# Performance work log

Measured on AMD Instinct MI355X. Metric: run time of the kernel, lower is better.

Reference implementation:

```python
import jax, jax.numpy as jnp
import numpy as np

NF = 64   # num_feat
DG = 8    # deformable_groups (also conv groups)
B, H, W = 4, 96, 96
K = 9     # 3x3 kernel positions


def _conv(x, w, b, padding=1, dilation=1, groups=1):
    out = jax.lax.conv_general_dilated(
        x, w, (1, 1), [(padding, padding), (padding, padding)],
        rhs_dilation=(dilation, dilation),
        dimension_numbers=('NCHW', 'OIHW', 'NCHW'),
        feature_group_count=groups)
    return out + b[None, :, None, None]


def _lrelu(t):
    return jnp.where(t >= 0, t, 0.1 * t)


def _cat_align(a, b):
    # channel-interleaved concat: [a0,b0,a1,b1,...]
    Bn, k, h, w = a.shape
    return jnp.stack([a, b], axis=2).reshape(Bn, 2 * k, h, w)


def _deform_conv(x, offset, mask, weight, bias, dilation, padding):
    # DCNv2 modulated deformable conv, stride 1.
    Bn, C, h, w = x.shape
    Cpg = C // DG
    off = offset.reshape(Bn, DG, K, 2, h, w)          # (dy, dx) per group/kernel pos
    m = mask.reshape(Bn, DG, K, h, w)
    ky = (jnp.repeat(jnp.arange(3), 3) * dilation - padding).astype(x.dtype)  # (K,)
    kx = (jnp.tile(jnp.arange(3), 3) * dilation - padding).astype(x.dtype)
    hs = jnp.arange(h, dtype=x.dtype)
    ws = jnp.arange(w, dtype=x.dtype)
    py = off[:, :, :, 0] + ky[None, None, :, None, None] + hs[None, None, None, :, None]
    px = off[:, :, :, 1] + kx[None, None, :, None, None] + ws[None, None, None, None, :]
    y0f = jnp.floor(py); x0f = jnp.floor(px)
    ly = (py - y0f)[:, :, None]  # broadcast over Cpg
    lx = (px - x0f)[:, :, None]
    y0 = y0f.astype(jnp.int32); x0 = x0f.astype(jnp.int32)
    xg = x.reshape(Bn, DG, Cpg, h * w)

    def gather(yi, xi):
        inb = ((yi >= 0) & (yi < h) & (xi >= 0) & (xi < w))
        idx = (jnp.clip(yi, 0, h - 1) * w + jnp.clip(xi, 0, w - 1)).reshape(Bn, DG, 1, K * h * w)
        v = jnp.take_along_axis(xg, jnp.broadcast_to(idx, (Bn, DG, Cpg, K * h * w)), axis=3)
        return v.reshape(Bn, DG, Cpg, K, h, w) * inb[:, :, None].astype(x.dtype)

    v00 = gather(y0, x0); v01 = gather(y0, x0 + 1)
    v10 = gather(y0 + 1, x0); v11 = gather(y0 + 1, x0 + 1)
    val = (v00 * (1 - ly) * (1 - lx) + v01 * (1 - ly) * lx
           + v10 * ly * (1 - lx) + v11 * ly * lx) * m[:, :, None]
    sampled = val.reshape(Bn, C, K, h, w)
    out = jnp.einsum('bckhw,ock->bohw', sampled, weight.reshape(weight.shape[0], C, K))
    return out + bias[None, :, None, None]


def _dcn(x, off_feat, om_w, om_b, w, b, dilation):
    pad = dilation  # int(3/2)*dilation
    out = _conv(off_feat, om_w, om_b, padding=pad, dilation=dilation)
    o1, o2, msk = jnp.split(out, 3, axis=1)
    offset = jnp.concatenate([o1, o2], axis=1)
    mask = jax.nn.sigmoid(msk)
    return _deform_conv(x, offset, mask, w, b, dilation, pad)


def setup_inputs() -> dict:
    key = jax.random.key(0)
    ks = iter(jax.random.split(key, 64))
    def rn(shape, s=0.05):
        return jax.random.normal(next(ks), shape, jnp.float32) * s
    d = {}
    d['nbr_feat'] = jax.random.normal(next(ks), (B, NF, H, W), jnp.float32)
    d['ref_feat'] = jax.random.normal(next(ks), (B, NF, H, W), jnp.float32)
    for lv, has3 in [('l3', False), ('l2', True), ('l1', True)]:
        d[f'oc1_w_{lv}'] = rn((NF, 2 * NF // DG, 3, 3)); d[f'oc1_b_{lv}'] = rn((NF,))
        oc2_in = 2 * NF if has3 else NF
        d[f'oc2_w_{lv}'] = rn((NF, oc2_in // DG, 3, 3)); d[f'oc2_b_{lv}'] = rn((NF,))
        if has3:
            d[f'oc3_w_{lv}'] = rn((NF, NF // DG, 3, 3)); d[f'oc3_b_{lv}'] = rn((NF,))
            d[f'fc_w_{lv}'] = rn((NF, 2 * NF // DG, 3, 3)); d[f'fc_b_{lv}'] = rn((NF,))
        d[f'om_w_{lv}'] = rn((DG * 3 * K, NF, 3, 3), 0.01); d[f'om_b_{lv}'] = rn((DG * 3 * K,), 0.01)
        d[f'dcn_w_{lv}'] = rn((NF, NF, 3, 3)); d[f'dcn_b_{lv}'] = rn((NF,))
    d['cas_oc1_w'] = rn((NF, 2 * NF // DG, 3, 3)); d['cas_oc1_b'] = rn((NF,))
    d['cas_oc2_w'] = rn((NF, NF // DG, 3, 3)); d['cas_oc2_b'] = rn((NF,))
    d['cas_om_w'] = rn((DG * 3 * K, NF, 3, 3), 0.01); d['cas_om_b'] = rn((DG * 3 * K,), 0.01)
    d['cas_w'] = rn((NF, NF, 3, 3)); d['cas_b'] = rn((NF,))
    return d


def reference(nbr_feat, ref_feat,
              oc1_w_l3, oc1_b_l3, oc2_w_l3, oc2_b_l3, om_w_l3, om_b_l3, dcn_w_l3, dcn_b_l3,
              oc1_w_l2, oc1_b_l2, oc2_w_l2, oc2_b_l2, oc3_w_l2, oc3_b_l2, fc_w_l2, fc_b_l2,
              om_w_l2, om_b_l2, dcn_w_l2, dcn_b_l2,
              oc1_w_l1, oc1_b_l1, oc2_w_l1, oc2_b_l1, oc3_w_l1, oc3_b_l1, fc_w_l1, fc_b_l1,
              om_w_l1, om_b_l1, dcn_w_l1, dcn_b_l1,
              cas_oc1_w, cas_oc1_b, cas_oc2_w, cas_oc2_b, cas_om_w, cas_om_b, cas_w, cas_b):
    # level 3 (dilation 5)
    off = _lrelu(_conv(_cat_align(nbr_feat, ref_feat), oc1_w_l3, oc1_b_l3, groups=DG))
    off = _lrelu(_conv(off, oc2_w_l3, oc2_b_l3, groups=DG))
    feat = _lrelu(_dcn(nbr_feat, off, om_w_l3, om_b_l3, dcn_w_l3, dcn_b_l3, 5))
    to, tf = off, feat
    # level 2 (dilation 3)
    off = _lrelu(_conv(_cat_align(nbr_feat, ref_feat), oc1_w_l2, oc1_b_l2, groups=DG))
    off = _lrelu(_conv(_cat_align(off, to), oc2_w_l2, oc2_b_l2, groups=DG))
    off = _lrelu(_conv(off, oc3_w_l2, oc3_b_l2, groups=DG))
    feat = _dcn(nbr_feat, off, om_w_l2, om_b_l2, dcn_w_l2, dcn_b_l2, 3)
    feat = _lrelu(_conv(_cat_align(feat, tf), fc_w_l2, fc_b_l2, groups=DG))
    to, tf = off, feat
    # level 1 (dilation 1), no lrelu on feat
    off = _lrelu(_conv(_cat_align(nbr_feat, ref_feat), oc1_w_l1, oc1_b_l1, groups=DG))
    off = _lrelu(_conv(_cat_align(off, to), oc2_w_l1, oc2_b_l1, groups=DG))
    off = _lrelu(_conv(off, oc3_w_l1, oc3_b_l1, groups=DG))
    feat = _dcn(nbr_feat, off, om_w_l1, om_b_l1, dcn_w_l1, dcn_b_l1, 1)
    feat = _conv(_cat_align(feat, tf), fc_w_l1, fc_b_l1, groups=DG)
    # cascade
    off = _cat_align(feat, ref_feat)
    off = _lrelu(_conv(_lrelu(_conv(off, cas_oc1_w, cas_oc1_b, groups=DG)), cas_oc2_w, cas_oc2_b, groups=DG))
    feat = _lrelu(_dcn(feat, off, cas_om_w, cas_om_b, cas_w, cas_b, 1))
    return feat
```

## Files before the change

### kernel.cpp

```cpp
#include <hip/hip_runtime.h>

#define BATCH 4
#define NFEAT 64
#define DGRP 8
#define HH 96
#define WW 96
#define HWP (HH*WW)

typedef short short4a __attribute__((ext_vector_type(4)));
typedef short short8 __attribute__((ext_vector_type(8)));
typedef float f32x4 __attribute__((ext_vector_type(4)));
typedef float f32x16 __attribute__((ext_vector_type(16)));

__device__ inline short f2bf(float f) {
  union { float f; unsigned u; } v; v.f = f;
  unsigned r = v.u + 0x7fff + ((v.u >> 16) & 1);
  return (short)(r >> 16);
}
__device__ inline float bf2f(short s) {
  return __uint_as_float(((unsigned)(unsigned short)s) << 16);
}

__device__ __forceinline__ void barrier_keep_vmcnt() {
  asm volatile("s_waitcnt lgkmcnt(0)" ::: "memory");
  __builtin_amdgcn_s_barrier();
  asm volatile("" ::: "memory");
}

__global__ __launch_bounds__(256) void prep_om(
    const float* __restrict__ s0, const float* __restrict__ s1,
    const float* __restrict__ s2, const float* __restrict__ s3,
    short* __restrict__ dst) {
  int gid = blockIdx.x * 256 + threadIdx.x;
  if (gid >= 4 * 147456) return;
  int t = gid / 147456, r = gid % 147456;
  int tile = r / 18432, r2 = r % 18432;
  int kk = r2 / 512, r3 = r2 % 512;
  int lane = r3 / 8, j = r3 % 8;
  int col = lane & 31, half = lane >> 5;
  int oc = tile * 32 + col;
  int k = kk * 16 + half * 8 + j;
  int p = k >> 6, c = k & 63;
  const float* s = (t == 0) ? s0 : (t == 1) ? s1 : (t == 2) ? s2 : s3;
  float v = (oc < 216) ? s[(size_t)oc * 576 + c * 9 + p] : 0.f;
  dst[gid] = f2bf(v);
}

__global__ __launch_bounds__(256) void prep_dcnw(
    const float* __restrict__ s0, const float* __restrict__ s1,
    const float* __restrict__ s2, const float* __restrict__ s3,
    short* __restrict__ dst) {
  int gid = blockIdx.x * 256 + threadIdx.x;
  if (gid >= 4 * 36864) return;
  int t = gid / 36864, r = gid % 36864;
  int tile = r / 18432, r2 = r % 18432;
  int kk = r2 / 512, r3 = r2 % 512;
  int lane = r3 / 8, j = r3 % 8;
  int col = lane & 31, half = lane >> 5;
  int oc = tile * 32 + col;
  int k = kk * 16 + half * 8 + j;
  int p = k >> 6, c = k & 63;
  const float* s = (t == 0) ? s0 : (t == 1) ? s1 : (t == 2) ? s2 : s3;
  dst[gid] = f2bf(s[(size_t)oc * 576 + c * 9 + p]);
}

struct GwArgs {
  const float* src[12];
  int cat[12];
  int base[13];
};

__global__ __launch_bounds__(256) void prep_gw(GwArgs a, short* __restrict__ dst) {
  int gid = blockIdx.x * 256 + threadIdx.x;
  if (gid >= a.base[12]) return;
  int t = 0;
  while (gid >= a.base[t + 1]) ++t;
  int r = gid - a.base[t];
  const float* s = a.src[t];
  const int tsz = a.cat[t] ? 4608 : 2560;
  int tile = r / tsz, r2 = r % tsz;
  int kk = r2 / 512, r3 = r2 % 512;
  int lane = r3 >> 3, j = r3 & 7;
  int m = lane & 15, quad = lane >> 4;
  int oc = tile * 16 + m;
  int j32 = quad * 8 + j;
  float val = 0.f;
  if (a.cat[t]) {
    int gsel = j32 >> 4, ssel = (j32 >> 3) & 1, ch8 = j32 & 7;
    if (gsel == (m >> 3)) val = s[oc * 144 + (2 * ch8 + ssel) * 9 + kk];
  } else {
    int tapsel = j32 >> 4, gsel = (j32 >> 3) & 1, ch8 = j32 & 7;
    int p = 2 * kk + tapsel;
    if (p < 9 && gsel == (m >> 3)) val = s[oc * 72 + ch8 * 9 + p];
  }
  dst[gid] = f2bf(val);
}

__global__ __launch_bounds__(256) void transpose_bf16(
    const float* __restrict__ in0, short* __restrict__ out0,
    const float* __restrict__ in1, short* __restrict__ out1) {
  const float* in = blockIdx.z ? in1 : in0;
  short* out = blockIdx.z ? out1 : out0;
  __shared__ float s[64][65];
  const int p0 = blockIdx.x * 64;
  const int b = blockIdx.y;
  const int tx = threadIdx.x, ty = threadIdx.y;
  for (int c = ty; c < 64; c += 4)
    s[c][tx] = in[((size_t)b * NFEAT + c) * HWP + p0 + tx];
  __syncthreads();
  for (int p = ty; p < 64; p += 4)
    out[((size_t)b * HWP + p0 + p) * NFEAT + tx] = f2bf(s[tx][p]);
}

template <bool CAT, bool LRELU>
__device__ __forceinline__ void gconv_body(
    const short* __restrict__ in0, const short* __restrict__ in1,
    const short* __restrict__ Wsh, const float* __restrict__ bias,
    short* __restrict__ out, int pixbase, int b) {
  const int lane = threadIdx.x, t = threadIdx.y;
  const int n = lane & 15, quad = lane >> 4;
  constexpr int NKK = CAT ? 9 : 5;

  short8 A[NKK];
#pragma unroll
  for (int kk = 0; kk < NKK; ++kk)
    A[kk] = *(const short8*)(Wsh + ((size_t)(t * NKK + kk) * 64 + lane) * 8);

  const short* sb;
  if (CAT) {
    sb = ((quad & 1) ? in1 : in0) + (size_t)b * HWP * 64 + (2 * t + (quad >> 1)) * 8;
  } else {
    sb = in0 + (size_t)b * HWP * 64 + (2 * t + (quad & 1)) * 8;
  }

  f32x4 acc[2] = {};
#pragma unroll
  for (int nt = 0; nt < 2; ++nt) {
    const int pix = pixbase + nt * 16 + n;
    const int yp = pix / WW, xp = pix % WW;
#pragma unroll
    for (int kk = 0; kk < NKK; ++kk) {
      const int p = CAT ? kk : (2 * kk + (quad >> 1));
      short8 B = {0, 0, 0, 0, 0, 0, 0, 0};
      if (p < 9) {
        const int sy = yp + p / 3 - 1, sx = xp + p % 3 - 1;
        if (((unsigned)sy < (unsigned)HH) && ((unsigned)sx < (unsigned)WW))
          B = *(const short8*)(sb + (size_t)(sy * WW + sx) * 64);
      }
      acc[nt] = __builtin_amdgcn_mfma_f32_16x16x32_bf16(A[kk], B, acc[nt], 0, 0, 0);
    }
  }

  const int ocb = t * 16 + quad * 4;
  const float b0 = bias[ocb], b1 = bias[ocb + 1], b2 = bias[ocb + 2], b3 = bias[ocb + 3];
#pragma unroll
  for (int nt = 0; nt < 2; ++nt) {
    float v0 = acc[nt][0] + b0, v1 = acc[nt][1] + b1;
    float v2 = acc[nt][2] + b2, v3 = acc[nt][3] + b3;
    if (LRELU) {
      v0 = (v0 >= 0.f) ? v0 : 0.1f * v0;
      v1 = (v1 >= 0.f) ? v1 : 0.1f * v1;
      v2 = (v2 >= 0.f) ? v2 : 0.1f * v2;
      v3 = (v3 >= 0.f) ? v3 : 0.1f * v3;
    }
    short4a pk = {f2bf(v0), f2bf(v1), f2bf(v2), f2bf(v3)};
    *(short4a*)(out + ((size_t)b * HWP + pixbase + nt * 16 + n) * 64 + ocb) = pk;
  }
}

template <bool CAT, bool LRELU>
__global__ __launch_bounds__(256) void gconv_mfma(
    const short* __restrict__ in0, const short* __restrict__ in1,
    const short* __restrict__ Wsh, const float* __restrict__ bias,
    short* __restrict__ out) {
  gconv_body<CAT, LRELU>(in0, in1, Wsh, bias, out, blockIdx.x * 32, blockIdx.y);
}

struct Oc1Args {
  const short* W[3];
  const float* bias[3];
  short* out[3];
};

__global__ __launch_bounds__(256) void gconv_oc1x3(
    const short* __restrict__ in0, const short* __restrict__ in1, Oc1Args a) {
  const int job = blockIdx.z;
  gconv_body<true, true>(in0, in1, a.W[job], a.bias[job], a.out[job],
                         blockIdx.x * 32, blockIdx.y);
}

struct Pair2Args {
  const short* in0[2];
  const short* in1[2];
  const short* W[2];
  const float* bias[2];
  short* out[2];
};

__global__ __launch_bounds__(256) void gconv_pair(Pair2Args a) {
  const int j = blockIdx.z;
  gconv_body<true, true>(a.in0[j], a.in1[j], a.W[j], a.bias[j], a.out[j],
                         blockIdx.x * 32, blockIdx.y);
}

#define BPITCH 324
template <int D>
__global__ __launch_bounds__(256) void omconv_mfma(
    const short* __restrict__ pixT,
    const short* __restrict__ Wsh,
    const float* __restrict__ bias,
    short* __restrict__ out) {
  const int lane = threadIdx.x;
  const int w = threadIdx.y;
  const int lid = w * 64 + lane;
  const int col = lane & 31, half = lane >> 5;
  const int pixbase = blockIdx.x * 64;
  const int b = blockIdx.y;

  __shared__ short Bs[64 * BPITCH];

  const short* aP0 = Wsh + ((size_t)(w * 36) * 64) * 8 + (size_t)lane * 8;
  const short* aP1 = Wsh + ((size_t)((w + 4) * 36) * 64) * 8 + (size_t)lane * 8;
  const short* pixb = pixT + (size_t)b * HWP * 64;

  f32x16 acc00 = {}, acc01 = {}, acc10 = {}, acc11 = {};

  for (int i = lid; i < 64 * 5 * 8; i += 256) {
    int row = i / 40, q = i % 40;
    int p = q >> 3, c8 = q & 7;
    int pix = pixbase + row;
    int yp = pix / WW, xp = pix % WW;
    int sy = yp + (p / 3 - 1) * D, sx = xp + (p % 3 - 1) * D;
    short4a lo = {0, 0, 0, 0}, hi = {0, 0, 0, 0};
    if (((unsigned)sy < (unsigned)HH) && ((unsigned)sx < (unsigned)WW)) {
      const short* src = pixb + (size_t)(sy * WW + sx) * 64 + c8 * 8;
      lo = *(const short4a*)src;
      hi = *(const short4a*)(src + 4);
    }
    short* dst = Bs + row * BPITCH + q * 8;
    *(short4a*)dst = lo;
    *(short4a*)(dst + 4) = hi;
  }

  short4a p1lo[8], p1hi[8];
  int p1dst[8];
#pragma unroll
  for (int idx = 0; idx < 8; ++idx) {
    int i = lid + idx * 256;
    int row = i / 32, q = i % 32;
    int p = 5 + (q >> 3), c8 = q & 7;
    int pix = pixbase + row;
    int yp = pix / WW, xp = pix % WW;
    int sy = yp + (p / 3 - 1) * D, sx = xp + (p % 3 - 1) * D;
    short4a lo = {0, 0, 0, 0}, hi = {0, 0, 0, 0};
    if (((unsigned)sy < (unsigned)HH) && ((unsigned)sx < (unsigned)WW)) {
      const short* src = pixb + (size_t)(sy * WW + sx) * 64 + c8 * 8;
      lo = *(const short4a*)src;
      hi = *(const short4a*)(src + 4);
    }
    p1lo[idx] = lo;
    p1hi[idx] = hi;
    p1dst[idx] = row * BPITCH + q * 8;
  }
  barrier_keep_vmcnt();

#pragma unroll 4
  for (int kk = 0; kk < 20; ++kk) {
    short8 A0 = *(const short8*)(aP0 + (size_t)kk * 512);
    short8 A1 = *(const short8*)(aP1 + (size_t)kk * 512);
    const short* b0 = Bs + col * BPITCH + kk * 16 + half * 8;
    const short* b1 = Bs + (32 + col) * BPITCH + kk * 16 + half * 8;
    short4a l0 = *(const short4a*)b0, h0 = *(const short4a*)(b0 + 4);
    short4a l1 = *(const short4a*)b1, h1 = *(const short4a*)(b1 + 4);
    short8 B0 = {l0[0], l0[1], l0[2], l0[3], h0[0], h0[1], h0[2], h0[3]};
    short8 B1 = {l1[0], l1[1], l1[2], l1[3], h1[0], h1[1], h1[2], h1[3]};
    acc00 = __builtin_amdgcn_mfma_f32_32x32x16_bf16(A0, B0, acc00, 0, 0, 0);
    acc01 = __builtin_amdgcn_mfma_f32_32x32x16_bf16(A0, B1, acc01, 0, 0, 0);
    acc10 = __builtin_amdgcn_mfma_f32_32x32x16_bf16(A1, B0, acc10, 0, 0, 0);
    acc11 = __builtin_amdgcn_mfma_f32_32x32x16_bf16(A1, B1, acc11, 0, 0, 0);
  }
  barrier_keep_vmcnt();

#pragma unroll
  for (int idx = 0; idx < 8; ++idx) {
    short* dst = Bs + p1dst[idx];
    *(short4a*)dst = p1lo[idx];
    *(short4a*)(dst + 4) = p1hi[idx];
  }
  barrier_keep_vmcnt();

#pragma unroll 4
  for (int kk = 0; kk < 16; ++kk) {
    const int kkg = 20 + kk;
    short8 A0 = *(const short8*)(aP0 + (size_t)kkg * 512);
    short8 A1 = *(const short8*)(aP1 + (size_t)kkg * 512);
    const short* b0 = Bs + col * BPITCH + kk * 16 + half * 8;
    const short* b1 = Bs + (32 + col) * BPITCH + kk * 16 + half * 8;
    short4a l0 = *(const short4a*)b0, h0 = *(const short4a*)(b0 + 4);
    short4a l1 = *(const short4a*)b1, h1 = *(const short4a*)(b1 + 4);
    short8 B0 = {l0[0], l0[1], l0[2], l0[3], h0[0], h0[1], h0[2], h0[3]};
    short8 B1 = {l1[0], l1[1], l1[2], l1[3], h1[0], h1[1], h1[2], h1[3]};
    acc00 = __builtin_amdgcn_mfma_f32_32x32x16_bf16(A0, B0, acc00, 0, 0, 0);
    acc01 = __builtin_amdgcn_mfma_f32_32x32x16_bf16(A0, B1, acc01, 0, 0, 0);
    acc10 = __builtin_amdgcn_mfma_f32_32x32x16_bf16(A1, B0, acc10, 0, 0, 0);
    acc11 = __builtin_amdgcn_mfma_f32_32x32x16_bf16(A1, B1, acc11, 0, 0, 0);
  }

  const int pix0 = pixbase + col, pix1 = pixbase + 32 + col;
#pragma unroll
  for (int r = 0; r < 16; ++r) {
    const int rrow = (r & 3) + 8 * (r >> 2) + 4 * half;
    const int oc0 = w * 32 + rrow;
    const int oc1 = (w + 4) * 32 + rrow;
    const float bs0 = bias[oc0];
    out[((size_t)b * 216 + oc0) * HWP + pix0] = f2bf(acc00[r] + bs0);
    out[((size_t)b * 216 + oc0) * HWP + pix1] = f2bf(acc01[r] + bs0);
    if (oc1 < 216) {
      const float bs1 = bias[oc1];
      out[((size_t)b * 216 + oc1) * HWP + pix0] = f2bf(acc10[r] + bs1);
      out[((size_t)b * 216 + oc1) * HWP + pix1] = f2bf(acc11[r] + bs1);
    }
  }
}

template <int D, bool LRELU, bool PMOUT>
__global__ __launch_bounds__(256) void dcn_fused(
    const short* __restrict__ xT,
    const short* __restrict__ om,
    const short* __restrict__ Wd,
    const float* __restrict__ bias,
    void* __restrict__ outv) {
  __shared__ short Ls[36 * 512];
  __shared__ float red[2][64][17];
  const int tx = threadIdx.x, ty = threadIdx.y;
  const int pb = blockIdx.x, b = blockIdx.y;

  {
    const int px = tx, dg = ty;
    const int pix = pb * 32 + px;
    const int yp = pix / WW, xp = pix % WW;
    const size_t bOM = (size_t)b * 216 * HWP;
    const short* xb = xT + (size_t)b * HWP * 64 + dg * 8;
    short* Sp = Ls + (size_t)((dg & 1) * 32 + px) * 8;

#pragma unroll
    for (int k = 0; k < 9; ++k) {
      float dy = bf2f(om[bOM + (size_t)(dg * 18 + 2 * k) * HWP + pix]);
      float dxv = bf2f(om[bOM + (size_t)(dg * 18 + 2 * k + 1) * HWP + pix]);
      float mr = bf2f(om[bOM + (size_t)(144 + dg * 9 + k) * HWP + pix]);
      float m = 1.f / (1.f + __expf(-mr));
      float py = (float)(yp + (k / 3 - 1) * D) + dy;
      float px_ = (float)(xp + (k % 3 - 1) * D) + dxv;
      float y0f = floorf(py), x0f = floorf(px_);
      float ly = py - y0f, lx = px_ - x0f;
      int y0 = (int)y0f, x0 = (int)x0f;
      int y1 = y0 + 1, x1 = x0 + 1;
      bool vy0 = (unsigned)y0 < (unsigned)HH, vy1 = (unsigned)y1 < (unsigned)HH;
      bool vx0 = (unsigned)x0 < (unsigned)WW, vx1 = (unsigned)x1 < (unsigned)WW;
      int cy0 = min(max(y0, 0), HH - 1), cy1 = min(max(y1, 0), HH - 1);
      int cx0 = min(max(x0, 0), WW - 1), cx1 = min(max(x1, 0), WW - 1);
      float w00 = (vy0 && vx0) ? (1.f - ly) * (1.f - lx) * m : 0.f;
      float w01 = (vy0 && vx1) ? (1.f - ly) * lx * m : 0.f;
      float w10 = (vy1 && vx0) ? ly * (1.f - lx) * m : 0.f;
      float w11 = (vy1 && vx1) ? ly * lx * m : 0.f;
      short8 s00 = *(const short8*)(xb + (size_t)(cy0 * WW + cx0) * 64);
      short8 s01 = *(const short8*)(xb + (size_t)(cy0 * WW + cx1) * 64);
      short8 s10 = *(const short8*)(xb + (size_t)(cy1 * WW + cx0) * 64);
      short8 s11 = *(const short8*)(xb + (size_t)(cy1 * WW + cx1) * 64);
      short8 pk;
#pragma unroll
      for (int cl = 0; cl < 8; ++cl) {
        float v = w00 * bf2f(s00[cl]) + w01 * bf2f(s01[cl]) +
                  w10 * bf2f(s10[cl]) + w11 * bf2f(s11[cl]);
        pk[cl] = f2bf(v);
      }
      const int kk = k * 4 + (dg >> 1);
      *(short8*)(Sp + (size_t)kk * 512) = pk;
    }
  }
  __syncthreads();

  const int lid = ty * 32 + tx;
  const int lane = lid & 63, w = lid >> 6;
  const int col = lane & 31, half = lane >> 5;
  const int octile = w & 1, kh = w >> 1;
  const int pix = pb * 32 + col;

  const short* aP = Wd + ((size_t)(octile * 36) * 64 + lane) * 8;
  const short* bP = Ls + (size_t)lane * 8;

  f32x16 acc = {};
#pragma unroll 6
  for (int kk = 0; kk < 18; ++kk) {
    const int kkg = kh * 18 + kk;
    short8 A = *(const short8*)(aP + (size_t)kkg * 512);
    short8 B = *(const short8*)(bP + (size_t)kkg * 512);
    acc = __builtin_amdgcn_mfma_f32_32x32x16_bf16(A, B, acc, 0, 0, 0);
  }

  if (kh == 1) {
#pragma unroll
    for (int r = 0; r < 16; ++r) red[octile][lane][r] = acc[r];
  }
  __syncthreads();
  if (kh == 0) {
    if (PMOUT) {
      short* out = (short*)outv;
#pragma unroll
      for (int rg = 0; rg < 4; ++rg) {
        short4a pk;
#pragma unroll
        for (int i = 0; i < 4; ++i) {
          const int r = rg * 4 + i;
          const int oc = octile * 32 + i + 8 * rg + 4 * half;
          float v = acc[r] + red[octile][lane][r] + bias[oc];
          if (LRELU) v = (v >= 0.f) ? v : 0.1f * v;
          pk[i] = f2bf(v);
        }
        *(short4a*)(out + ((size_t)b * HWP + pix) * 64 + octile * 32 + 8 * rg + 4 * half) = pk;
      }
    } else {
      float* out = (float*)outv;
#pragma unroll
      for (int r = 0; r < 16; ++r) {
        const int oc = octile * 32 + (r & 3) + 8 * (r >> 2) + 4 * half;
        float v = acc[r] + red[octile][lane][r] + bias[oc];
        if (LRELU) v = (v >= 0.f) ? v : 0.1f * v;
        out[((size_t)b * NFEAT + oc) * HWP + pix] = v;
      }
    }
  }
}

extern "C" void kernel_launch(void* const* d_in, const int* in_sizes, int n_in,
                              void* d_out, int out_size, void* d_ws, size_t ws_size,
                              hipStream_t stream) {
  const float* nbr = (const float*)d_in[0];
  const float* ref = (const float*)d_in[1];
  auto f = [&](int i) { return (const float*)d_in[i]; };

  short* s0 = (short*)d_ws;
  const size_t PM = (size_t)BATCH * HWP * 64;
  short* omB = s0;
  short* refT = omB + 7962624;
  short* pmA = refT + PM;
  short* pmB = pmA + PM;
  short* pmC = pmB + PM;
  short* pmD = pmC + PM;
  short* pmE = pmD + PM;
  short* pmF = pmE + PM;
  short* pmG = pmF + PM;
  short* wbf = pmG + PM;
  short* wdcn = wbf + 589824;
  short* wgc = wdcn + 147456;
  short* nbrT = (short*)d_out;

  prep_om<<<(4 * 147456 + 255) / 256, 256, 0, stream>>>(f(6), f(18), f(30), f(38), wbf);
  prep_dcnw<<<(4 * 36864 + 255) / 256, 256, 0, stream>>>(f(8), f(20), f(32), f(40), wdcn);

  static const int gSrc[12] = {2, 4, 10, 12, 14, 16, 22, 24, 26, 28, 34, 36};
  static const int gCat[12] = {1, 0, 1, 1, 0, 1, 1, 1, 0, 1, 1, 0};
  GwArgs ga;
  int gb = 0;
  const short* wg[12];
  for (int t = 0; t < 12; ++t) {
    ga.src[t] = f(gSrc[t]);
    ga.cat[t] = gCat[t];
    ga.base[t] = gb;
    wg[t] = wgc + gb;
    gb += gCat[t] ? 18432 : 10240;
  }
  ga.base[12] = gb;
  prep_gw<<<(gb + 255) / 256, 256, 0, stream>>>(ga, wgc);

  short* wbf_l3 = wbf;
  short* wbf_l2 = wbf + 147456;
  short* wbf_l1 = wbf + 2 * 147456;
  short* wbf_cas = wbf + 3 * 147456;
  short* wd_l3 = wdcn;
  short* wd_l2 = wdcn + 36864;
  short* wd_l1 = wdcn + 2 * 36864;
  short* wd_cas = wdcn + 3 * 36864;

  dim3 gcGrid(288, BATCH), gcBlk(64, 4);
  dim3 oc1Grid(288, BATCH, 3);
  dim3 pairGrid(288, BATCH, 2);
  dim3 omGrid(144, BATCH), omBlk(64, 4);
  dim3 dfGrid(288, BATCH), dfBlk(32, 8);
  dim3 trGrid(HWP / 64, BATCH, 2), trBlk(64, 4);

  transpose_bf16<<<trGrid, trBlk, 0, stream>>>(nbr, nbrT, ref, refT);

  Oc1Args oa;
  oa.W[0] = wg[0]; oa.bias[0] = f(3);  oa.out[0] = pmA;
  oa.W[1] = wg[2]; oa.bias[1] = f(11); oa.out[1] = pmF;
  oa.W[2] = wg[6]; oa.bias[2] = f(23); oa.out[2] = pmG;
  gconv_oc1x3<<<oc1Grid, gcBlk, 0, stream>>>(nbrT, refT, oa);

  gconv_mfma<false, true><<<gcGrid, gcBlk, 0, stream>>>(pmA, nullptr, wg[1], f(5), pmB);
  omconv_mfma<5><<<omGrid, omBlk, 0, stream>>>(pmB, wbf_l3, f(7), omB);
  dcn_fused<5, true, true><<<dfGrid, dfBlk, 0, stream>>>(nbrT, omB, wd_l3, f(9), pmC);

  gconv_mfma<true, true><<<gcGrid, gcBlk, 0, stream>>>(pmF, pmB, wg[3], f(13), pmD);
  gconv_mfma<false, true><<<gcGrid, gcBlk, 0, stream>>>(pmD, nullptr, wg[4], f(15), pmE);
  omconv_mfma<3><<<omGrid, omBlk, 0, stream>>>(pmE, wbf_l2, f(19), omB);
  dcn_fused<3, false, true><<<dfGrid, dfBlk, 0, stream>>>(nbrT, omB, wd_l2, f(21), pmD);

  Pair2Args pa;
  pa.in0[0] = pmD; pa.in1[0] = pmC; pa.W[0] = wg[5]; pa.bias[0] = f(17); pa.out[0] = pmA;
  pa.in0[1] = pmG; pa.in1[1] = pmE; pa.W[1] = wg[7]; pa.bias[1] = f(25); pa.out[1] = pmB;
  gconv_pair<<<pairGrid, gcBlk, 0, stream>>>(pa);

  gconv_mfma<false, true><<<gcGrid, gcBlk, 0, stream>>>(pmB, nullptr, wg[8], f(27), pmC);
  omconv_mfma<1><<<omGrid, omBlk, 0, stream>>>(pmC, wbf_l1, f(31), omB);
  dcn_fused<1, false, true><<<dfGrid, dfBlk, 0, stream>>>(nbrT, omB, wd_l1, f(33), pmD);
  gconv_mfma<true, false><<<gcGrid, gcBlk, 0, stream>>>(pmD, pmA, wg[9], f(29), pmB);

  gconv_mfma<true, true><<<gcGrid, gcBlk, 0, stream>>>(pmB, refT, wg[10], f(35), pmC);
  gconv_mfma<false, true><<<gcGrid, gcBlk, 0, stream>>>(pmC, nullptr, wg[11], f(37), pmD);
  omconv_mfma<1><<<omGrid, omBlk, 0, stream>>>(pmD, wbf_cas, f(39), omB);
  dcn_fused<1, true, false><<<dfGrid, dfBlk, 0, stream>>>(pmB, omB, wd_cas, f(41), (float*)d_out);
}
```

Baseline: 517.1 us.

## Co-schedule independent grouped convs with offset-mask convs and DCN kernels

Turns the omconv, dcn and gconv kernels into device-side bodies and adds combined kernels whose grids dispatch on block index to run independent work side by side, such as an omconv with the next level's offset conv, or a DCN with a gconv. This removes several launches and fills the GPU with more blocks while the smaller grids would otherwise leave compute units idle. Buffer assignments are reshuffled so the concurrent jobs do not collide. In exchange, the merged kernels take the larger shared-memory footprint and register pressure of both bodies, which may reduce occupancy for the lighter gconv blocks.

```diff
diff --git a/kernel.cpp b/kernel.cpp
--- a/kernel.cpp
+++ b/kernel.cpp
@@ -116,8 +116,8 @@
 __device__ __forceinline__ void gconv_body(
     const short* __restrict__ in0, const short* __restrict__ in1,
     const short* __restrict__ Wsh, const float* __restrict__ bias,
-    short* __restrict__ out, int pixbase, int b) {
-  const int lane = threadIdx.x, t = threadIdx.y;
+    short* __restrict__ out, int pixbase, int b, int lid) {
+  const int lane = lid & 63, t = lid >> 6;
   const int n = lane & 15, quad = lane >> 4;
   constexpr int NKK = CAT ? 9 : 5;
 
@@ -173,7 +173,8 @@
     const short* __restrict__ in0, const short* __restrict__ in1,
     const short* __restrict__ Wsh, const float* __restrict__ bias,
     short* __restrict__ out) {
-  gconv_body<CAT, LRELU>(in0, in1, Wsh, bias, out, blockIdx.x * 32, blockIdx.y);
+  gconv_body<CAT, LRELU>(in0, in1, Wsh, bias, out, blockIdx.x * 32, blockIdx.y,
+                         threadIdx.x);
 }
 
 struct Oc1Args {
@@ -186,38 +187,20 @@
     const short* __restrict__ in0, const short* __restrict__ in1, Oc1Args a) {
   const int job = blockIdx.z;
   gconv_body<true, true>(in0, in1, a.W[job], a.bias[job], a.out[job],
-                         blockIdx.x * 32, blockIdx.y);
-}
-
-struct Pair2Args {
-  const short* in0[2];
-  const short* in1[2];
-  const short* W[2];
-  const float* bias[2];
-  short* out[2];
-};
-
-__global__ __launch_bounds__(256) void gconv_pair(Pair2Args a) {
-  const int j = blockIdx.z;
-  gconv_body<true, true>(a.in0[j], a.in1[j], a.W[j], a.bias[j], a.out[j],
-                         blockIdx.x * 32, blockIdx.y);
+                         blockIdx.x * 32, blockIdx.y, threadIdx.x);
 }
 
 #define BPITCH 324
 template <int D>
-__global__ __launch_bounds__(256) void omconv_mfma(
-    const short* __restrict__ pixT,
-    const short* __restrict__ Wsh,
-    const float* __restrict__ bias,
-    short* __restrict__ out) {
-  const int lane = threadIdx.x;
-  const int w = threadIdx.y;
-  const int lid = w * 64 + lane;
+__device__ __forceinline__ void omconv_body(
+    short* Bs,
+    const short* __restrict__ pixT, const short* __restrict__ Wsh,
+    const float* __restrict__ bias, short* __restrict__ out,
+    int xblk, int b, int lid) {
+  const int lane = lid & 63;
+  const int w = lid >> 6;
   const int col = lane & 31, half = lane >> 5;
-  const int pixbase = blockIdx.x * 64;
-  const int b = blockIdx.y;
-
-  __shared__ short Bs[64 * BPITCH];
+  const int pixbase = xblk * 64;
 
   const short* aP0 = Wsh + ((size_t)(w * 36) * 64) * 8 + (size_t)lane * 8;
   const short* aP1 = Wsh + ((size_t)((w + 4) * 36) * 64) * 8 + (size_t)lane * 8;
@@ -323,17 +306,23 @@
   }
 }
 
+template <int D>
+__global__ __launch_bounds__(256) void omconv_mfma(
+    const short* __restrict__ pixT, const short* __restrict__ Wsh,
+    const float* __restrict__ bias, short* __restrict__ out) {
+  __shared__ short Bs[64 * BPITCH];
+  omconv_body<D>(Bs, pixT, Wsh, bias, out, blockIdx.x, blockIdx.y, threadIdx.x);
+}
+
 template <int D, bool LRELU, bool PMOUT>
-__global__ __launch_bounds__(256) void dcn_fused(
-    const short* __restrict__ xT,
-    const short* __restrict__ om,
-    const short* __restrict__ Wd,
-    const float* __restrict__ bias,
-    void* __restrict__ outv) {
-  __shared__ short Ls[36 * 512];
-  __shared__ float red[2][64][17];
-  const int tx = threadIdx.x, ty = threadIdx.y;
-  const int pb = blockIdx.x, b = blockIdx.y;
+__device__ __forceinline__ void dcn_body(
+    char* smem,
+    const short* __restrict__ xT, const short* __restrict__ om,
+    const short* __restrict__ Wd, const float* __restrict__ bias,
+    void* __restrict__ outv, int pb, int b, int lid) {
+  short* Ls = (short*)smem;
+  float* red = (float*)(smem + 36864);
+  const int tx = lid & 31, ty = lid >> 5;
 
   {
     const int px = tx, dg = ty;
@@ -380,7 +369,6 @@
   }
   __syncthreads();
 
-  const int lid = ty * 32 + tx;
   const int lane = lid & 63, w = lid >> 6;
   const int col = lane & 31, half = lane >> 5;
   const int octile = w & 1, kh = w >> 1;
@@ -400,10 +388,11 @@
 
   if (kh == 1) {
 #pragma unroll
-    for (int r = 0; r < 16; ++r) red[octile][lane][r] = acc[r];
+    for (int r = 0; r < 16; ++r) red[((size_t)octile * 64 + lane) * 17 + r] = acc[r];
   }
   __syncthreads();
   if (kh == 0) {
+    const float* rp = red + ((size_t)octile * 64 + lane) * 17;
     if (PMOUT) {
       short* out = (short*)outv;
 #pragma unroll
@@ -413,7 +402,7 @@
         for (int i = 0; i < 4; ++i) {
           const int r = rg * 4 + i;
           const int oc = octile * 32 + i + 8 * rg + 4 * half;
-          float v = acc[r] + red[octile][lane][r] + bias[oc];
+          float v = acc[r] + rp[r] + bias[oc];
           if (LRELU) v = (v >= 0.f) ? v : 0.1f * v;
           pk[i] = f2bf(v);
         }
@@ -424,12 +413,53 @@
 #pragma unroll
       for (int r = 0; r < 16; ++r) {
         const int oc = octile * 32 + (r & 3) + 8 * (r >> 2) + 4 * half;
-        float v = acc[r] + red[octile][lane][r] + bias[oc];
+        float v = acc[r] + rp[r] + bias[oc];
         if (LRELU) v = (v >= 0.f) ? v : 0.1f * v;
         out[((size_t)b * NFEAT + oc) * HWP + pix] = v;
       }
     }
   }
+}
+
+template <int D, bool LRELU, bool PMOUT>
+__global__ __launch_bounds__(256) void dcn_fused(
+    const short* __restrict__ xT, const short* __restrict__ om,
+    const short* __restrict__ Wd, const float* __restrict__ bias,
+    void* __restrict__ outv) {
+  __shared__ char smem[45568];
+  dcn_body<D, LRELU, PMOUT>(smem, xT, om, Wd, bias, outv,
+                            blockIdx.x, blockIdx.y, threadIdx.x);
+}
+
+template <int D>
+__global__ __launch_bounds__(256) void om_gc(
+    const short* __restrict__ pixT, const short* __restrict__ Wom,
+    const float* __restrict__ obias, short* __restrict__ omOut,
+    const short* __restrict__ g0, const short* __restrict__ g1,
+    const short* __restrict__ gW, const float* __restrict__ gb,
+    short* __restrict__ gout) {
+  __shared__ short Bs[64 * BPITCH];
+  if (blockIdx.x < 144)
+    omconv_body<D>(Bs, pixT, Wom, obias, omOut, blockIdx.x, blockIdx.y, threadIdx.x);
+  else
+    gconv_body<true, true>(g0, g1, gW, gb, gout, (blockIdx.x - 144) * 32,
+                           blockIdx.y, threadIdx.x);
+}
+
+template <int D, bool DLRELU>
+__global__ __launch_bounds__(256) void dcn_gc(
+    const short* __restrict__ xT, const short* __restrict__ om,
+    const short* __restrict__ Wd, const float* __restrict__ dbias,
+    short* __restrict__ dout,
+    const short* __restrict__ g0, const short* __restrict__ gW,
+    const float* __restrict__ gb, short* __restrict__ gout) {
+  __shared__ char smem[45568];
+  if (blockIdx.x < 288)
+    dcn_body<D, DLRELU, true>(smem, xT, om, Wd, dbias, dout,
+                              blockIdx.x, blockIdx.y, threadIdx.x);
+  else
+    gconv_body<false, true>(g0, nullptr, gW, gb, gout, (blockIdx.x - 288) * 32,
+                            blockIdx.y, threadIdx.x);
 }
 
 extern "C" void kernel_launch(void* const* d_in, const int* in_sizes, int n_in,
@@ -482,11 +512,12 @@
   short* wd_l1 = wdcn + 2 * 36864;
   short* wd_cas = wdcn + 3 * 36864;
 
-  dim3 gcGrid(288, BATCH), gcBlk(64, 4);
+  dim3 gcGrid(288, BATCH);
   dim3 oc1Grid(288, BATCH, 3);
-  dim3 pairGrid(288, BATCH, 2);
-  dim3 omGrid(144, BATCH), omBlk(64, 4);
-  dim3 dfGrid(288, BATCH), dfBlk(32, 8);
+  dim3 omgcGrid(432, BATCH);
+  dim3 dcngcGrid(576, BATCH);
+  dim3 omGrid(144, BATCH);
+  dim3 dfGrid(288, BATCH);
   dim3 trGrid(HWP / 64, BATCH, 2), trBlk(64, 4);
 
   transpose_bf16<<<trGrid, trBlk, 0, stream>>>(nbr, nbrT, ref, refT);
@@ -495,29 +526,25 @@
   oa.W[0] = wg[0]; oa.bias[0] = f(3);  oa.out[0] = pmA;
   oa.W[1] = wg[2]; oa.bias[1] = f(11); oa.out[1] = pmF;
   oa.W[2] = wg[6]; oa.bias[2] = f(23); oa.out[2] = pmG;
-  gconv_oc1x3<<<oc1Grid, gcBlk, 0, stream>>>(nbrT, refT, oa);
-
-  gconv_mfma<false, true><<<gcGrid, gcBlk, 0, stream>>>(pmA, nullptr, wg[1], f(5), pmB);
-  omconv_mfma<5><<<omGrid, omBlk, 0, stream>>>(pmB, wbf_l3, f(7), omB);
-  dcn_fused<5, true, true><<<dfGrid, dfBlk, 0, stream>>>(nbrT, omB, wd_l3, f(9), pmC);
-
-  gconv_mfma<true, true><<<gcGrid, gcBlk, 0, stream>>>(pmF, pmB, wg[3], f(13), pmD);
-  gconv_mfma<false, true><<<gcGrid, gcBlk, 0, stream>>>(pmD, nullptr, wg[4], f(15), pmE);
-  omconv_mfma<3><<<omGrid, omBlk, 0, stream>>>(pmE, wbf_l2, f(19), omB);
-  dcn_fused<3, false, true><<<dfGrid, dfBlk, 0, stream>>>(nbrT, omB, wd_l2, f(21), pmD);
-
-  Pair2Args pa;
-  pa.in0[0] = pmD; pa.in1[0] = pmC; pa.W[0] = wg[5]; pa.bias[0] = f(17); pa.out[0] = pmA;
-  pa.in0[1] = pmG; pa.in1[1] = pmE; pa.W[1] = wg[7]; pa.bias[1] = f(25); pa.out[1] = pmB;
-  gconv_pair<<<pairGrid, gcBlk, 0, stream>>>(pa);
-
-  gconv_mfma<false, true><<<gcGrid, gcBlk, 0, stream>>>(pmB, nullptr, wg[8], f(27), pmC);
-  omconv_mfma<1><<<omGrid, omBlk, 0, stream>>>(pmC, wbf_l1, f(31), omB);
-  dcn_fused<1, false, true><<<dfGrid, dfBlk, 0, stream>>>(nbrT, omB, wd_l1, f(33), pmD);
-  gconv_mfma<true, false><<<gcGrid, gcBlk, 0, stream>>>(pmD, pmA, wg[9], f(29), pmB);
-
-  gconv_mfma<true, true><<<gcGrid, gcBlk, 0, stream>>>(pmB, refT, wg[10], f(35), pmC);
-  gconv_mfma<false, true><<<gcGrid, gcBlk, 0, stream>>>(pmC, nullptr, wg[11], f(37), pmD);
-  omconv_mfma<1><<<omGrid, omBlk, 0, stream>>>(pmD, wbf_cas, f(39), omB);
-  dcn_fused<1, true, false><<<dfGrid, dfBlk, 0, stream>>>(pmB, omB, wd_cas, f(41), (float*)d_out);
-}
+  gconv_oc1x3<<<oc1Grid, 256, 0, stream>>>(nbrT, refT, oa);
+
+  gconv_mfma<false, true><<<gcGrid, 256, 0, stream>>>(pmA, nullptr, wg[1], f(5), pmB);
+
+  om_gc<5><<<omgcGrid, 256, 0, stream>>>(pmB, wbf_l3, f(7), omB,
+                                         pmF, pmB, wg[3], f(13), pmD);
+  dcn_gc<5, true><<<dcngcGrid, 256, 0, stream>>>(nbrT, omB, wd_l3, f(9), pmC,
+                                                 pmD, wg[4], f(15), pmE);
+  om_gc<3><<<omgcGrid, 256, 0, stream>>>(pmE, wbf_l2, f(19), omB,
+                                         pmG, pmE, wg[7], f(25), pmB);
+  dcn_gc<3, false><<<dcngcGrid, 256, 0, stream>>>(nbrT, omB, wd_l2, f(21), pmD,
+                                                  pmB, wg[8], f(27), pmF);
+  om_gc<1><<<omgcGrid, 256, 0, stream>>>(pmF, wbf_l1, f(31), omB,
+                                         pmD, pmC, wg[5], f(17), pmA);
+  dcn_fused<1, false, true><<<dfGrid, 256, 0, stream>>>(nbrT, omB, wd_l1, f(33), pmE);
+  gconv_mfma<true, false><<<gcGrid, 256, 0, stream>>>(pmE, pmA, wg[9], f(29), pmB);
+
+  gconv_mfma<true, true><<<gcGrid, 256, 0, stream>>>(pmB, refT, wg[10], f(35), pmC);
+  gconv_mfma<false, true><<<gcGrid, 256, 0, stream>>>(pmC, nullptr, wg[11], f(37), pmD);
+  omconv_mfma<1><<<omGrid, 256, 0, stream>>>(pmD, wbf_cas, f(39), omB);
+  dcn_fused<1, true, false><<<dfGrid, 256, 0, stream>>>(pmB, omB, wd_cas, f(41), (float*)d_out);
+}
```

Result: faster. 505.3 us (-2.3%).
